# Performance work log

Measured on AMD Instinct MI355X. Metric: run time of the kernel, lower is better.

Reference implementation:

```python
import jax, jax.numpy as jnp
import numpy as np

S, B, D, H, E, K, FF = 1024, 8, 768, 12, 8, 2, 3072


def _ln(x, w, b, eps=1e-5):
    m = x.mean(-1, keepdims=True)
    v = ((x - m) ** 2).mean(-1, keepdims=True)
    return (x - m) / jnp.sqrt(v + eps) * w + b


def setup_inputs() -> dict:
    key = jax.random.key(0)
    ks = jax.random.split(key, 12)
    s = 0.02
    return {
        "x": jax.random.normal(ks[0], (S, B, D), dtype=jnp.float32),
        "ln1_w": jnp.ones((D,), jnp.float32),
        "ln1_b": jnp.zeros((D,), jnp.float32),
        "in_proj_w": jax.random.normal(ks[1], (3 * D, D), jnp.float32) * s,
        "in_proj_b": jnp.zeros((3 * D,), jnp.float32),
        "out_proj_w": jax.random.normal(ks[2], (D, D), jnp.float32) * s,
        "out_proj_b": jnp.zeros((D,), jnp.float32),
        "ln2_w": jnp.ones((D,), jnp.float32),
        "ln2_b": jnp.zeros((D,), jnp.float32),
        "gate_w": jax.random.normal(ks[3], (E, D), jnp.float32) * s,
        "w1": jax.random.normal(ks[4], (E, D, FF), jnp.float32) * s,
        "b1": jnp.zeros((E, FF), jnp.float32),
        "w2": jax.random.normal(ks[5], (E, FF, D), jnp.float32) * s,
        "b2": jnp.zeros((E, D), jnp.float32),
    }


def reference(x, ln1_w, ln1_b, in_proj_w, in_proj_b, out_proj_w, out_proj_b,
              ln2_w, ln2_b, gate_w, w1, b1, w2, b2):
    s, b, d = x.shape
    hd = d // H
    # --- self attention (nn.MultiheadAttention, seq-first, no mask) ---
    h = _ln(x, ln1_w, ln1_b)
    qkv = h @ in_proj_w.T + in_proj_b            # [S, B, 3D]
    q, k, v = jnp.split(qkv, 3, axis=-1)

    def heads(t):
        return t.reshape(s, b, H, hd).transpose(1, 2, 0, 3)  # [B, H, S, hd]

    q, k, v = heads(q) * (hd ** -0.5), heads(k), heads(v)
    att = jax.nn.softmax(jnp.einsum('bhqd,bhkd->bhqk', q, k), axis=-1)
    o = jnp.einsum('bhqk,bhkd->bhqd', att, v).transpose(2, 0, 1, 3).reshape(s, b, d)
    o = o @ out_proj_w.T + out_proj_b
    x = x + o
    # --- MoE FFN ---
    h2 = _ln(x, ln2_w, ln2_b)
    tok = h2.reshape(-1, d)                      # [T, D], T = S*B
    logits = tok @ gate_w.T                      # [T, E]
    rw = jax.nn.softmax(logits.astype(jnp.float32), axis=-1)
    rw_top, sel = jax.lax.top_k(rw, K)           # [T, K]
    rw_top = rw_top / rw_top.sum(-1, keepdims=True)
    rw_top = rw_top.astype(tok.dtype)
    out = jnp.zeros_like(tok)
    for e in range(E):  # small fixed expert loop; math matches gather/scatter dispatch
        we = jnp.where(sel == e, rw_top, 0.0).sum(-1)       # [T] combine weight
        mid = tok @ w1[e] + b1[e]
        mid = mid * jax.nn.sigmoid(1.702 * mid)              # QuickGELU
        out = out + we[:, None] * (mid @ w2[e] + b2[e])
    return x + out.reshape(s, b, d), logits
```

## Files before the change

### kernel.cpp

```cpp
#include <hip/hip_runtime.h>
#include <stdint.h>

#define S_LEN  1024
#define BATCH  8
#define DMODEL 768
#define NHEAD  12
#define HDIM   64
#define NEXP   8
#define FFDIM  3072
#define NTOK   8192
#define D3     2304
#define NGATH  16384
#define MAXWL  136

typedef unsigned short u16;
typedef unsigned int   u32;
typedef __attribute__((ext_vector_type(8))) short bf16x8;
typedef __attribute__((ext_vector_type(4))) float f32x4;
typedef __attribute__((ext_vector_type(4))) short s16x4;

__device__ __forceinline__ u16 f2bf(float f){
  u32 x = __float_as_uint(f);
  x += 0x7fffu + ((x >> 16) & 1u);
  return (u16)(x >> 16);
}
__device__ __forceinline__ float bf2f(u16 u){
  return __uint_as_float(((u32)u) << 16);
}
__device__ __forceinline__ void gl_lds16(const void* g, void* l){
  __builtin_amdgcn_global_load_lds(
      (const __attribute__((address_space(1))) u32*)(uintptr_t)g,
      (__attribute__((address_space(3))) u32*)(u32)(uintptr_t)l,
      16, 0, 0);
}
__device__ __forceinline__ int swz64(int r){ return ((r & 7) ^ ((r >> 3) & 7)) << 4; }

__global__ __launch_bounds__(256)
void cvt_bf16(const float* __restrict__ in, u16* __restrict__ out, int n)
{
  int i = (blockIdx.x * 256 + threadIdx.x) * 4;
  if (i + 3 < n) {
    float4 v = *(const float4*)(in + i);
    out[i]     = f2bf(v.x);
    out[i + 1] = f2bf(v.y);
    out[i + 2] = f2bf(v.z);
    out[i + 3] = f2bf(v.w);
  }
}

__global__ __launch_bounds__(256)
void transpose_cvt(const float* __restrict__ in, u16* __restrict__ out, int rows, int cols)
{
  __shared__ float tile[32][33];
  const size_t eo = (size_t)blockIdx.z * rows * cols;
  in  += eo; out += eo;
  const int bx = blockIdx.x * 32, by = blockIdx.y * 32;
  const int tx = threadIdx.x, ty = threadIdx.y;
  #pragma unroll
  for (int i = 0; i < 4; i++)
    tile[ty + i * 8][tx] = in[(size_t)(by + ty + i * 8) * cols + bx + tx];
  __syncthreads();
  #pragma unroll
  for (int i = 0; i < 4; i++)
    out[(size_t)(bx + ty + i * 8) * rows + by + tx] = f2bf(tile[tx][ty + i * 8]);
}

__global__ __launch_bounds__(256)
void ln_fwd(const float* __restrict__ x, const float* __restrict__ w, const float* __restrict__ b,
            u16* __restrict__ out)
{
  const int t = blockIdx.x, tid = threadIdx.x;
  const float* xr = x + (size_t)t * DMODEL;
  const float v0 = xr[tid], v1 = xr[tid + 256], v2 = xr[tid + 512];
  float s = v0 + v1 + v2, ss = v0 * v0 + v1 * v1 + v2 * v2;
  #pragma unroll
  for (int d = 1; d < 64; d <<= 1) { s += __shfl_xor(s, d); ss += __shfl_xor(ss, d); }
  __shared__ float rs[4], rq[4];
  if ((tid & 63) == 0) { rs[tid >> 6] = s; rq[tid >> 6] = ss; }
  __syncthreads();
  s  = rs[0] + rs[1] + rs[2] + rs[3];
  ss = rq[0] + rq[1] + rq[2] + rq[3];
  const float mean = s * (1.f / DMODEL);
  const float rstd = rsqrtf(ss * (1.f / DMODEL) - mean * mean + 1e-5f);
  u16* orow = out + (size_t)t * DMODEL;
  orow[tid]       = f2bf((v0 - mean) * rstd * w[tid]       + b[tid]);
  orow[tid + 256] = f2bf((v1 - mean) * rstd * w[tid + 256] + b[tid + 256]);
  orow[tid + 512] = f2bf((v2 - mean) * rstd * w[tid + 512] + b[tid + 512]);
}

__global__ __launch_bounds__(256)
void ln2_gate(const float* __restrict__ x1, const float* __restrict__ w, const float* __restrict__ b,
              const float* __restrict__ gate_w, u16* __restrict__ h2,
              float* __restrict__ logits, float* __restrict__ selw, int* __restrict__ seli)
{
  const int t = blockIdx.x, tid = threadIdx.x;
  const float* xr = x1 + (size_t)t * DMODEL;
  const float v0 = xr[tid], v1 = xr[tid + 256], v2 = xr[tid + 512];
  float s = v0 + v1 + v2, ss = v0 * v0 + v1 * v1 + v2 * v2;
  #pragma unroll
  for (int d = 1; d < 64; d <<= 1) { s += __shfl_xor(s, d); ss += __shfl_xor(ss, d); }
  __shared__ float rs[4], rq[4];
  if ((tid & 63) == 0) { rs[tid >> 6] = s; rq[tid >> 6] = ss; }
  __syncthreads();
  s  = rs[0] + rs[1] + rs[2] + rs[3];
  ss = rq[0] + rq[1] + rq[2] + rq[3];
  const float mean = s * (1.f / DMODEL);
  const float rstd = rsqrtf(ss * (1.f / DMODEL) - mean * mean + 1e-5f);
  __shared__ float row[DMODEL];
  const float y0 = (v0 - mean) * rstd * w[tid]       + b[tid];
  const float y1 = (v1 - mean) * rstd * w[tid + 256] + b[tid + 256];
  const float y2 = (v2 - mean) * rstd * w[tid + 512] + b[tid + 512];
  row[tid] = y0; row[tid + 256] = y1; row[tid + 512] = y2;
  u16* hr = h2 + (size_t)t * DMODEL;
  hr[tid] = f2bf(y0); hr[tid + 256] = f2bf(y1); hr[tid + 512] = f2bf(y2);
  __syncthreads();
  __shared__ float lg[NEXP];
  if (tid < 64) {
    const int e = tid >> 3, j = tid & 7;
    const float* gw = gate_w + e * DMODEL;
    float a = 0.f;
    for (int d = j; d < DMODEL; d += 8) a += row[d] * gw[d];
    a += __shfl_xor(a, 1); a += __shfl_xor(a, 2); a += __shfl_xor(a, 4);
    if (j == 0) lg[e] = a;
  }
  __syncthreads();
  if (tid < NEXP) logits[(size_t)t * NEXP + tid] = lg[tid];
  if (tid == 0) {
    int ia = 0, ib = -1;
    float va = -1e30f, vb = -1e30f;
    #pragma unroll
    for (int e = 0; e < NEXP; e++) {
      const float p = lg[e];
      if (p > va)      { vb = va; ib = ia; va = p; ia = e; }
      else if (p > vb) { vb = p; ib = e; }
    }
    const float pb = __expf(vb - va);
    const float inv = 1.f / (1.f + pb);
    selw[2 * t]     = inv;
    selw[2 * t + 1] = pb * inv;
    seli[2 * t]     = ia;
    seli[2 * t + 1] = ib;
  }
}

__global__ __launch_bounds__(256)
void route_count(const int* __restrict__ seli, int* __restrict__ blkcnt)
{
  __shared__ int c[NEXP];
  const int tid = threadIdx.x;
  if (tid < NEXP) c[tid] = 0;
  __syncthreads();
  const int t = blockIdx.x * 256 + tid;
  atomicAdd(&c[seli[2 * t]], 1);
  atomicAdd(&c[seli[2 * t + 1]], 1);
  __syncthreads();
  if (tid < NEXP) blkcnt[blockIdx.x * NEXP + tid] = c[tid];
}

__global__ void route_scan(const int* __restrict__ blkcnt, int* __restrict__ offs,
                           int* __restrict__ blkbase, int* __restrict__ wl, int* __restrict__ nwork)
{
  const int tid = threadIdx.x;
  __shared__ int tot[NEXP];
  __shared__ int off_s[NEXP + 1];
  if (tid < NEXP) {
    int s = 0;
    for (int blk = 0; blk < 32; blk++) s += blkcnt[blk * NEXP + tid];
    tot[tid] = s;
  }
  __syncthreads();
  if (tid == 0) {
    int run = 0;
    for (int e = 0; e < NEXP; e++) { off_s[e] = run; run += tot[e]; }
    off_s[NEXP] = run;
    int nw = 0;
    for (int e = 0; e < NEXP; e++) {
      const int nb = (tot[e] + 127) >> 7;
      for (int i2 = 0; i2 < nb; i2++) wl[nw++] = (e << 16) | i2;
    }
    nwork[0] = nw;
  }
  __syncthreads();
  if (tid <= NEXP) offs[tid] = off_s[tid];
  if (tid < NEXP) {
    int run = off_s[tid];
    for (int blk = 0; blk < 32; blk++) { blkbase[blk * NEXP + tid] = run; run += blkcnt[blk * NEXP + tid]; }
  }
}

__global__ __launch_bounds__(256)
void route_place(const int* __restrict__ seli, const int* __restrict__ blkbase,
                 int* __restrict__ perm, int* __restrict__ posmap)
{
  __shared__ int cnts[2][4][NEXP];
  __shared__ int base[NEXP];
  const int tid = threadIdx.x, l = tid & 63, w = tid >> 6, blk = blockIdx.x;
  const int t = blk * 256 + tid;
  const unsigned long long ltm = (1ull << l) - 1ull;
  int my_e[2], my_r[2];
  my_e[0] = seli[2 * t]; my_e[1] = seli[2 * t + 1];
  my_r[0] = 0; my_r[1] = 0;
  if (tid < NEXP) base[tid] = blkbase[blk * NEXP + tid];
  #pragma unroll
  for (int k = 0; k < 2; k++) {
    #pragma unroll
    for (int ee = 0; ee < NEXP; ee++) {
      const unsigned long long msk = __ballot(my_e[k] == ee);
      if (my_e[k] == ee) my_r[k] = (int)__popcll(msk & ltm);
      if (l == ee) cnts[k][w][ee] = (int)__popcll(msk);
    }
  }
  __syncthreads();
  #pragma unroll
  for (int k = 0; k < 2; k++) {
    const int e = my_e[k];
    int pre = base[e];
    for (int k2 = 0; k2 < 2; k2++)
      for (int w2 = 0; w2 < 4; w2++)
        if (k2 < k || (k2 == k && w2 < w)) pre += cnts[k2][w2][e];
    const int pos = pre + my_r[k];
    perm[pos] = t;
    posmap[2 * t + k] = pos;
  }
}

template<int MODE>
__global__ __launch_bounds__(256)
void gemm128(const u16* __restrict__ A, const u16* __restrict__ Bw,
             int M, int N, int Kd,
             const float* __restrict__ bias, const float* __restrict__ resid,
             void* __restrict__ outp,
             const int* __restrict__ perm, const int* __restrict__ offs,
             const int* __restrict__ wl, const int* __restrict__ nwork)
{
  __shared__ u16 As[128 * 64];
  __shared__ u16 Bs[128 * 64];
  const int tid = threadIdx.x;
  const int l   = tid & 63;
  const int w   = tid >> 6;
  const int wm  = w >> 1, wn = w & 1;
  const int bn  = blockIdx.y;

  int gbase = 0, cnt = M, e = 0, bm = blockIdx.x;
  if (MODE >= 2) {
    if (blockIdx.x >= nwork[0]) return;
    const int wk = wl[blockIdx.x];
    e  = wk >> 16;
    bm = wk & 0xffff;
    gbase = offs[e];
    cnt   = offs[e + 1] - gbase;
  }
  const u16*   Bp = Bw   + (MODE >= 2 ? (size_t)e * N * Kd : 0);
  const float* bp = bias + (MODE >= 2 ? e * N : 0);

  int arow[4], acol[4], brow[4];
  #pragma unroll
  for (int i = 0; i < 4; i++) {
    const int c = tid + 256 * i;
    const int r = c >> 3;
    const int f = (r & 7) ^ ((r >> 3) & 7);
    acol[i] = ((c & 7) ^ f) * 8;
    brow[i] = bn * 128 + r;
    int g;
    if (MODE == 2)      { int gp = gbase + bm * 128 + r; if (gp > NGATH - 1) gp = NGATH - 1; g = perm[gp]; }
    else if (MODE == 3) { int gp = gbase + bm * 128 + r; if (gp > NGATH - 1) gp = NGATH - 1; g = gp; }
    else                g = bm * 128 + r;
    arow[i] = g;
  }

  f32x4 acc[4][4] = {};
  const int nk = Kd >> 6;
  for (int kt = 0; kt < nk; kt++) {
    const int kb = kt * 64;
    #pragma unroll
    for (int i = 0; i < 4; i++) {
      gl_lds16(A  + (size_t)arow[i] * Kd + kb + acol[i], &As[(i * 256 + w * 64) * 8]);
      gl_lds16(Bp + (size_t)brow[i] * Kd + kb + acol[i], &Bs[(i * 256 + w * 64) * 8]);
    }
    __syncthreads();
    #pragma unroll
    for (int ks = 0; ks < 2; ks++) {
      bf16x8 af[4], bv[4];
      #pragma unroll
      for (int m = 0; m < 4; m++) {
        const int row = wm * 64 + m * 16 + (l & 15);
        af[m] = *(const bf16x8*)((const char*)As +
                  ((row * 128 + ks * 64 + (l >> 4) * 16) ^ swz64(row)));
      }
      #pragma unroll
      for (int n = 0; n < 4; n++) {
        const int row = wn * 64 + n * 16 + (l & 15);
        bv[n] = *(const bf16x8*)((const char*)Bs +
                  ((row * 128 + ks * 64 + (l >> 4) * 16) ^ swz64(row)));
      }
      #pragma unroll
      for (int m = 0; m < 4; m++)
        #pragma unroll
        for (int n = 0; n < 4; n++)
          acc[m][n] = __builtin_amdgcn_mfma_f32_16x16x32_bf16(af[m], bv[n], acc[m][n], 0, 0, 0);
    }
    __syncthreads();
  }

  float bvl[4];
  int   coln[4];
  #pragma unroll
  for (int n = 0; n < 4; n++) { coln[n] = bn * 128 + wn * 64 + n * 16 + (l & 15); bvl[n] = bp[coln[n]]; }
  #pragma unroll
  for (int m = 0; m < 4; m++) {
    const int rb = bm * 128 + wm * 64 + m * 16 + ((l >> 4) << 2);
    #pragma unroll
    for (int n = 0; n < 4; n++) {
      #pragma unroll
      for (int r = 0; r < 4; r++) {
        const int row = rb + r;
        const float v = acc[m][n][r] + bvl[n];
        if (MODE == 0) {
          ((u16*)outp)[(size_t)row * N + coln[n]] = f2bf(v);
        } else if (MODE == 1) {
          ((float*)outp)[(size_t)row * N + coln[n]] = v + resid[(size_t)row * N + coln[n]];
        } else if (MODE == 2) {
          if (row < cnt) {
            const float gg = v / (1.f + __expf(-1.702f * v));
            ((u16*)outp)[(size_t)(gbase + row) * FFDIM + coln[n]] = f2bf(gg);
          }
        } else {
          if (row < cnt)
            ((u16*)outp)[(size_t)(gbase + row) * DMODEL + coln[n]] = f2bf(v);
        }
      }
    }
  }
}

__global__ __launch_bounds__(256)
void attn_fwd(const u16* __restrict__ qkv, u16* __restrict__ o)
{
  __shared__ u16 Ksw[64 * 64];
  __shared__ u16 Vt [64 * 64];
  __shared__ u16 Pl [4 * 16 * 64];
  const int tid = threadIdx.x;
  const int l   = tid & 63, w = tid >> 6;
  const int qt  = blockIdx.x;
  const int b_  = blockIdx.y / NHEAD;
  const int hh  = blockIdx.y % NHEAD;

  const int qrow = qt * 64 + w * 16 + (l & 15);
  const size_t qoff = ((size_t)(qrow * BATCH + b_)) * D3 + hh * HDIM + (l >> 4) * 8;
  const bf16x8 qa0 = *(const bf16x8*)&qkv[qoff];
  const bf16x8 qa1 = *(const bf16x8*)&qkv[qoff + 32];

  f32x4 oacc[4] = {};
  float m_[4], l_[4];
  #pragma unroll
  for (int r = 0; r < 4; r++) { m_[r] = -1e30f; l_[r] = 0.f; }

  u16* Pw = Pl + w * 1024;
  const int pswz = swz64(l & 15);

  for (int kt = 0; kt < 16; kt++) {
    #pragma unroll
    for (int i = 0; i < 2; i++) {
      const int c = tid + 256 * i;
      const int key = c >> 3, dimb = (c & 7) * 8;
      const size_t gb = ((size_t)((kt * 64 + key) * BATCH + b_)) * D3 + hh * HDIM + dimb;
      const bf16x8 kd = *(const bf16x8*)&qkv[gb + DMODEL];
      const bf16x8 vd = *(const bf16x8*)&qkv[gb + 2 * DMODEL];
      *(bf16x8*)((char*)Ksw + ((key * 128 + dimb * 2) ^ swz64(key))) = kd;
      #pragma unroll
      for (int j = 0; j < 8; j++) {
        const int dim = dimb + j;
        *(u16*)((char*)Vt + ((dim * 128 + key * 2) ^ swz64(dim))) = (u16)vd[j];
      }
    }
    __syncthreads();

    f32x4 sc[4] = {};
    #pragma unroll
    for (int kb2 = 0; kb2 < 4; kb2++) {
      const int key = kb2 * 16 + (l & 15);
      const int ksz = swz64(key);
      #pragma unroll
      for (int ks = 0; ks < 2; ks++) {
        const bf16x8 kf = *(const bf16x8*)((char*)Ksw +
            ((key * 128 + (ks * 32 + (l >> 4) * 8) * 2) ^ ksz));
        sc[kb2] = __builtin_amdgcn_mfma_f32_16x16x32_bf16(ks ? qa1 : qa0, kf, sc[kb2], 0, 0, 0);
      }
    }
    #pragma unroll
    for (int kb2 = 0; kb2 < 4; kb2++)
      #pragma unroll
      for (int r = 0; r < 4; r++) sc[kb2][r] *= 0.125f;

    float nm[4], corr[4], ps[4];
    #pragma unroll
    for (int r = 0; r < 4; r++) {
      float pm = fmaxf(fmaxf(sc[0][r], sc[1][r]), fmaxf(sc[2][r], sc[3][r]));
      pm = fmaxf(pm, __shfl_xor(pm, 1));
      pm = fmaxf(pm, __shfl_xor(pm, 2));
      pm = fmaxf(pm, __shfl_xor(pm, 4));
      pm = fmaxf(pm, __shfl_xor(pm, 8));
      nm[r]   = fmaxf(m_[r], pm);
      corr[r] = __expf(m_[r] - nm[r]);
      m_[r]   = nm[r];
      ps[r]   = 0.f;
    }
    #pragma unroll
    for (int kb2 = 0; kb2 < 4; kb2++) {
      #pragma unroll
      for (int r = 0; r < 4; r++) {
        const float p = __expf(sc[kb2][r] - nm[r]);
        ps[r] += p;
        const int prow = (l >> 4) * 4 + r;
        const int pcol = kb2 * 16 + (l & 15);
        *(u16*)((char*)Pw + ((prow * 128 + pcol * 2) ^ swz64(prow))) = f2bf(p);
      }
    }
    #pragma unroll
    for (int r = 0; r < 4; r++) {
      float s = ps[r];
      s += __shfl_xor(s, 1); s += __shfl_xor(s, 2);
      s += __shfl_xor(s, 4); s += __shfl_xor(s, 8);
      l_[r] = l_[r] * corr[r] + s;
      #pragma unroll
      for (int ob = 0; ob < 4; ob++) oacc[ob][r] *= corr[r];
    }

    #pragma unroll
    for (int ob = 0; ob < 4; ob++) {
      const int dim = ob * 16 + (l & 15);
      const int vsz = swz64(dim);
      #pragma unroll
      for (int ks = 0; ks < 2; ks++) {
        const int kko = (ks * 32 + (l >> 4) * 8) * 2;
        const bf16x8 pf = *(const bf16x8*)((char*)Pw + (((l & 15) * 128 + kko) ^ pswz));
        const bf16x8 vf = *(const bf16x8*)((char*)Vt + ((dim * 128 + kko) ^ vsz));
        oacc[ob] = __builtin_amdgcn_mfma_f32_16x16x32_bf16(pf, vf, oacc[ob], 0, 0, 0);
      }
    }
    __syncthreads();
  }

  #pragma unroll
  for (int r = 0; r < 4; r++) {
    const float inv = 1.f / l_[r];
    const int qs = qt * 64 + w * 16 + (l >> 4) * 4 + r;
    #pragma unroll
    for (int ob = 0; ob < 4; ob++)
      o[((size_t)(qs * BATCH + b_)) * DMODEL + hh * HDIM + ob * 16 + (l & 15)] =
          f2bf(oacc[ob][r] * inv);
  }
}

__global__ __launch_bounds__(192)
void moe_combine(const float* __restrict__ x1, const u16* __restrict__ eout,
                 const int* __restrict__ posmap, const float* __restrict__ selw,
                 float* __restrict__ out)
{
  const int t = blockIdx.x, j = threadIdx.x;
  const int p0 = posmap[2 * t], p1 = posmap[2 * t + 1];
  const float w0 = selw[2 * t], w1 = selw[2 * t + 1];
  const float4 xv = ((const float4*)(x1 + (size_t)t * DMODEL))[j];
  const s16x4 a = ((const s16x4*)(eout + (size_t)p0 * DMODEL))[j];
  const s16x4 c = ((const s16x4*)(eout + (size_t)p1 * DMODEL))[j];
  float4 r;
  r.x = xv.x + w0 * bf2f((u16)a[0]) + w1 * bf2f((u16)c[0]);
  r.y = xv.y + w0 * bf2f((u16)a[1]) + w1 * bf2f((u16)c[1]);
  r.z = xv.z + w0 * bf2f((u16)a[2]) + w1 * bf2f((u16)c[2]);
  r.w = xv.w + w0 * bf2f((u16)a[3]) + w1 * bf2f((u16)c[3]);
  ((float4*)(out + (size_t)t * DMODEL))[j] = r;
}

#define MB (1ull << 20)
static const size_t OFF_H    = 0;
static const size_t OFF_QKV  = 16 * MB;
static const size_t OFF_O    = 54 * MB;
static const size_t OFF_IPW  = 67 * MB;
static const size_t OFF_OPW  = 71 * MB;
static const size_t OFF_MID  = 0;
static const size_t OFF_X1   = 101 * MB;
static const size_t OFF_H2   = 127 * MB;
static const size_t OFF_W1T  = 140 * MB;
static const size_t OFF_W2T  = 178 * MB;
static const size_t OFF_EOUT = 216 * MB;
static const size_t OFF_SELW = 242 * MB;
static const size_t OFF_PERM = 242 * MB + (1 << 16);
static const size_t OFF_POS  = 242 * MB + (2 << 16);
static const size_t OFF_SELI = 242 * MB + (3 << 16);
static const size_t OFF_BCNT = 242 * MB + (4 << 16);
static const size_t OFF_BBASE= 242 * MB + (4 << 16) + 4096;
static const size_t OFF_OFFS = 242 * MB + (4 << 16) + 8192;
static const size_t OFF_WL   = 242 * MB + (5 << 16);
static const size_t OFF_NW   = 242 * MB + (5 << 16) + 1024;

extern "C" void kernel_launch(void* const* d_in, const int* in_sizes, int n_in,
                              void* d_out, int out_size, void* d_ws, size_t ws_size,
                              hipStream_t stream)
{
  const float* x     = (const float*)d_in[0];
  const float* ln1w  = (const float*)d_in[1];
  const float* ln1b  = (const float*)d_in[2];
  const float* ipw_f = (const float*)d_in[3];
  const float* ipb   = (const float*)d_in[4];
  const float* opw_f = (const float*)d_in[5];
  const float* opb   = (const float*)d_in[6];
  const float* ln2w  = (const float*)d_in[7];
  const float* ln2b  = (const float*)d_in[8];
  const float* gatew = (const float*)d_in[9];
  const float* w1    = (const float*)d_in[10];
  const float* b1    = (const float*)d_in[11];
  const float* w2    = (const float*)d_in[12];
  const float* b2    = (const float*)d_in[13];

  char* ws = (char*)d_ws;
  u16*   h    = (u16*)(ws + OFF_H);
  u16*   qkv  = (u16*)(ws + OFF_QKV);
  u16*   ob   = (u16*)(ws + OFF_O);
  u16*   ipw  = (u16*)(ws + OFF_IPW);
  u16*   opw  = (u16*)(ws + OFF_OPW);
  u16*   mid  = (u16*)(ws + OFF_MID);
  float* x1   = (float*)(ws + OFF_X1);
  u16*   h2   = (u16*)(ws + OFF_H2);
  u16*   w1t  = (u16*)(ws + OFF_W1T);
  u16*   w2t  = (u16*)(ws + OFF_W2T);
  u16*   eout = (u16*)(ws + OFF_EOUT);
  float* selw = (float*)(ws + OFF_SELW);
  int*   perm = (int*)(ws + OFF_PERM);
  int*   posm = (int*)(ws + OFF_POS);
  int*   seli = (int*)(ws + OFF_SELI);
  int*   bcnt = (int*)(ws + OFF_BCNT);
  int*   bbas = (int*)(ws + OFF_BBASE);
  int*   offs = (int*)(ws + OFF_OFFS);
  int*   wl   = (int*)(ws + OFF_WL);
  int*   nwork= (int*)(ws + OFF_NW);
  float* outx  = (float*)d_out;
  float* outlg = outx + (size_t)NTOK * DMODEL;

  cvt_bf16<<<(D3 * DMODEL) / 1024, 256, 0, stream>>>(ipw_f, ipw, D3 * DMODEL);
  cvt_bf16<<<(DMODEL * DMODEL) / 1024, 256, 0, stream>>>(opw_f, opw, DMODEL * DMODEL);
  transpose_cvt<<<dim3(FFDIM / 32, DMODEL / 32, NEXP), dim3(32, 8), 0, stream>>>(w1, w1t, DMODEL, FFDIM);
  transpose_cvt<<<dim3(DMODEL / 32, FFDIM / 32, NEXP), dim3(32, 8), 0, stream>>>(w2, w2t, FFDIM, DMODEL);

  ln_fwd<<<NTOK, 256, 0, stream>>>(x, ln1w, ln1b, h);
  gemm128<0><<<dim3(NTOK / 128, D3 / 128, 1), 256, 0, stream>>>(
      h, ipw, NTOK, D3, DMODEL, ipb, nullptr, qkv, nullptr, nullptr, nullptr, nullptr);
  attn_fwd<<<dim3(S_LEN / 64, BATCH * NHEAD), 256, 0, stream>>>(qkv, ob);
  gemm128<1><<<dim3(NTOK / 128, DMODEL / 128, 1), 256, 0, stream>>>(
      ob, opw, NTOK, DMODEL, DMODEL, opb, x, x1, nullptr, nullptr, nullptr, nullptr);

  ln2_gate<<<NTOK, 256, 0, stream>>>(x1, ln2w, ln2b, gatew, h2, outlg, selw, seli);
  route_count<<<32, 256, 0, stream>>>(seli, bcnt);
  route_scan<<<1, 64, 0, stream>>>(bcnt, offs, bbas, wl, nwork);
  route_place<<<32, 256, 0, stream>>>(seli, bbas, perm, posm);

  gemm128<2><<<dim3(MAXWL, FFDIM / 128, 1), 256, 0, stream>>>(
      h2, w1t, NGATH, FFDIM, DMODEL, b1, nullptr, mid, perm, offs, wl, nwork);
  gemm128<3><<<dim3(MAXWL, DMODEL / 128, 1), 256, 0, stream>>>(
      mid, w2t, NGATH, DMODEL, FFDIM, b2, nullptr, eout, nullptr, offs, wl, nwork);

  moe_combine<<<NTOK, 192, 0, stream>>>(x1, eout, posm, selw, outx);
}
```

Baseline: 594.7 us.

## Enlarge GEMM tiles to 256x128 and vectorize epilogue stores

Doubles the M dimension of every GEMM block tile to 256 rows, so each warp computes a 128x64 sub-tile with 32 accumulators. Routing work lists are rebuilt in 256-row chunks to match, which halves the block count and the B-tile reloads. MFMA operands are swapped so each lane holds four consecutive output columns, which lets the epilogue use packed bf16 conversion and vector stores, and bias and residual become vector loads. The costs are higher register and LDS use, lower occupancy, and more padded rows wasted in the expert GEMMs.

```diff
diff --git a/kernel.cpp b/kernel.cpp
--- a/kernel.cpp
+++ b/kernel.cpp
@@ -11,7 +11,7 @@
 #define NTOK   8192
 #define D3     2304
 #define NGATH  16384
-#define MAXWL  136
+#define MAXWL  72
 
 typedef unsigned short u16;
 typedef unsigned int   u32;
@@ -26,6 +26,9 @@
 }
 __device__ __forceinline__ float bf2f(u16 u){
   return __uint_as_float(((u32)u) << 16);
+}
+__device__ __forceinline__ u32 pkbf(float a, float b){
+  u32 d; asm("v_cvt_pk_bf16_f32 %0, %1, %2" : "=v"(d) : "v"(a), "v"(b)); return d;
 }
 __device__ __forceinline__ void gl_lds16(const void* g, void* l){
   __builtin_amdgcn_global_load_lds(
@@ -175,7 +178,7 @@
     off_s[NEXP] = run;
     int nw = 0;
     for (int e = 0; e < NEXP; e++) {
-      const int nb = (tot[e] + 127) >> 7;
+      const int nb = (tot[e] + 255) >> 8;
       for (int i2 = 0; i2 < nb; i2++) wl[nw++] = (e << 16) | i2;
     }
     nwork[0] = nw;
@@ -226,14 +229,14 @@
 
 template<int MODE>
 __global__ __launch_bounds__(256)
-void gemm128(const u16* __restrict__ A, const u16* __restrict__ Bw,
+void gemm256(const u16* __restrict__ A, const u16* __restrict__ Bw,
              int M, int N, int Kd,
              const float* __restrict__ bias, const float* __restrict__ resid,
              void* __restrict__ outp,
              const int* __restrict__ perm, const int* __restrict__ offs,
              const int* __restrict__ wl, const int* __restrict__ nwork)
 {
-  __shared__ u16 As[128 * 64];
+  __shared__ u16 As[256 * 64];
   __shared__ u16 Bs[128 * 64];
   const int tid = threadIdx.x;
   const int l   = tid & 63;
@@ -253,40 +256,35 @@
   const u16*   Bp = Bw   + (MODE >= 2 ? (size_t)e * N * Kd : 0);
   const float* bp = bias + (MODE >= 2 ? e * N : 0);
 
-  int arow[4], acol[4], brow[4];
-  #pragma unroll
-  for (int i = 0; i < 4; i++) {
+  int arow[8], acol[8], brow[4];
+  #pragma unroll
+  for (int i = 0; i < 8; i++) {
     const int c = tid + 256 * i;
     const int r = c >> 3;
     const int f = (r & 7) ^ ((r >> 3) & 7);
     acol[i] = ((c & 7) ^ f) * 8;
-    brow[i] = bn * 128 + r;
     int g;
-    if (MODE == 2)      { int gp = gbase + bm * 128 + r; if (gp > NGATH - 1) gp = NGATH - 1; g = perm[gp]; }
-    else if (MODE == 3) { int gp = gbase + bm * 128 + r; if (gp > NGATH - 1) gp = NGATH - 1; g = gp; }
-    else                g = bm * 128 + r;
+    if (MODE == 2)      { int gp = gbase + bm * 256 + r; if (gp > NGATH - 1) gp = NGATH - 1; g = perm[gp]; }
+    else if (MODE == 3) { int gp = gbase + bm * 256 + r; if (gp > NGATH - 1) gp = NGATH - 1; g = gp; }
+    else                g = bm * 256 + r;
     arow[i] = g;
-  }
-
-  f32x4 acc[4][4] = {};
+    if (i < 4) brow[i] = bn * 128 + r;
+  }
+
+  f32x4 acc[8][4] = {};
   const int nk = Kd >> 6;
   for (int kt = 0; kt < nk; kt++) {
     const int kb = kt * 64;
     #pragma unroll
-    for (int i = 0; i < 4; i++) {
-      gl_lds16(A  + (size_t)arow[i] * Kd + kb + acol[i], &As[(i * 256 + w * 64) * 8]);
-      gl_lds16(Bp + (size_t)brow[i] * Kd + kb + acol[i], &Bs[(i * 256 + w * 64) * 8]);
+    for (int i = 0; i < 8; i++) {
+      gl_lds16(A + (size_t)arow[i] * Kd + kb + acol[i], &As[(tid + 256 * i) * 8]);
+      if (i < 4)
+        gl_lds16(Bp + (size_t)brow[i] * Kd + kb + acol[i], &Bs[(tid + 256 * i) * 8]);
     }
     __syncthreads();
     #pragma unroll
     for (int ks = 0; ks < 2; ks++) {
-      bf16x8 af[4], bv[4];
-      #pragma unroll
-      for (int m = 0; m < 4; m++) {
-        const int row = wm * 64 + m * 16 + (l & 15);
-        af[m] = *(const bf16x8*)((const char*)As +
-                  ((row * 128 + ks * 64 + (l >> 4) * 16) ^ swz64(row)));
-      }
+      bf16x8 bv[4];
       #pragma unroll
       for (int n = 0; n < 4; n++) {
         const int row = wn * 64 + n * 16 + (l & 15);
@@ -294,40 +292,51 @@
                   ((row * 128 + ks * 64 + (l >> 4) * 16) ^ swz64(row)));
       }
       #pragma unroll
-      for (int m = 0; m < 4; m++)
+      for (int m = 0; m < 8; m++) {
+        const int row = wm * 128 + m * 16 + (l & 15);
+        const bf16x8 af = *(const bf16x8*)((const char*)As +
+                  ((row * 128 + ks * 64 + (l >> 4) * 16) ^ swz64(row)));
         #pragma unroll
         for (int n = 0; n < 4; n++)
-          acc[m][n] = __builtin_amdgcn_mfma_f32_16x16x32_bf16(af[m], bv[n], acc[m][n], 0, 0, 0);
+          acc[m][n] = __builtin_amdgcn_mfma_f32_16x16x32_bf16(bv[n], af, acc[m][n], 0, 0, 0);
+      }
     }
     __syncthreads();
   }
 
-  float bvl[4];
-  int   coln[4];
-  #pragma unroll
-  for (int n = 0; n < 4; n++) { coln[n] = bn * 128 + wn * 64 + n * 16 + (l & 15); bvl[n] = bp[coln[n]]; }
-  #pragma unroll
-  for (int m = 0; m < 4; m++) {
-    const int rb = bm * 128 + wm * 64 + m * 16 + ((l >> 4) << 2);
+  f32x4 biasv[4];
+  int   c0[4];
+  #pragma unroll
+  for (int n = 0; n < 4; n++) {
+    c0[n] = bn * 128 + wn * 64 + n * 16 + ((l >> 4) << 2);
+    biasv[n] = *(const f32x4*)(bp + c0[n]);
+  }
+  #pragma unroll
+  for (int m = 0; m < 8; m++) {
+    const int row = bm * 256 + wm * 128 + m * 16 + (l & 15);
     #pragma unroll
     for (int n = 0; n < 4; n++) {
-      #pragma unroll
-      for (int r = 0; r < 4; r++) {
-        const int row = rb + r;
-        const float v = acc[m][n][r] + bvl[n];
-        if (MODE == 0) {
-          ((u16*)outp)[(size_t)row * N + coln[n]] = f2bf(v);
-        } else if (MODE == 1) {
-          ((float*)outp)[(size_t)row * N + coln[n]] = v + resid[(size_t)row * N + coln[n]];
-        } else if (MODE == 2) {
-          if (row < cnt) {
-            const float gg = v / (1.f + __expf(-1.702f * v));
-            ((u16*)outp)[(size_t)(gbase + row) * FFDIM + coln[n]] = f2bf(gg);
-          }
-        } else {
-          if (row < cnt)
-            ((u16*)outp)[(size_t)(gbase + row) * DMODEL + coln[n]] = f2bf(v);
+      f32x4 v = acc[m][n] + biasv[n];
+      if (MODE == 0) {
+        *(uint2*)((u16*)outp + (size_t)row * N + c0[n]) =
+            make_uint2(pkbf(v[0], v[1]), pkbf(v[2], v[3]));
+      } else if (MODE == 1) {
+        const size_t o = (size_t)row * N + c0[n];
+        f32x4 rv = *(const f32x4*)(resid + o);
+        v += rv;
+        *(f32x4*)((float*)outp + o) = v;
+      } else if (MODE == 2) {
+        if (row < cnt) {
+          #pragma unroll
+          for (int r = 0; r < 4; r++)
+            v[r] = v[r] * __builtin_amdgcn_rcpf(1.f + __expf(-1.702f * v[r]));
+          *(uint2*)((u16*)outp + (size_t)(gbase + row) * FFDIM + c0[n]) =
+              make_uint2(pkbf(v[0], v[1]), pkbf(v[2], v[3]));
         }
+      } else {
+        if (row < cnt)
+          *(uint2*)((u16*)outp + (size_t)(gbase + row) * DMODEL + c0[n]) =
+              make_uint2(pkbf(v[0], v[1]), pkbf(v[2], v[3]));
       }
     }
   }
@@ -542,10 +551,10 @@
   transpose_cvt<<<dim3(DMODEL / 32, FFDIM / 32, NEXP), dim3(32, 8), 0, stream>>>(w2, w2t, FFDIM, DMODEL);
 
   ln_fwd<<<NTOK, 256, 0, stream>>>(x, ln1w, ln1b, h);
-  gemm128<0><<<dim3(NTOK / 128, D3 / 128, 1), 256, 0, stream>>>(
+  gemm256<0><<<dim3(NTOK / 256, D3 / 128, 1), 256, 0, stream>>>(
       h, ipw, NTOK, D3, DMODEL, ipb, nullptr, qkv, nullptr, nullptr, nullptr, nullptr);
   attn_fwd<<<dim3(S_LEN / 64, BATCH * NHEAD), 256, 0, stream>>>(qkv, ob);
-  gemm128<1><<<dim3(NTOK / 128, DMODEL / 128, 1), 256, 0, stream>>>(
+  gemm256<1><<<dim3(NTOK / 256, DMODEL / 128, 1), 256, 0, stream>>>(
       ob, opw, NTOK, DMODEL, DMODEL, opb, x, x1, nullptr, nullptr, nullptr, nullptr);
 
   ln2_gate<<<NTOK, 256, 0, stream>>>(x1, ln2w, ln2b, gatew, h2, outlg, selw, seli);
@@ -553,9 +562,9 @@
   route_scan<<<1, 64, 0, stream>>>(bcnt, offs, bbas, wl, nwork);
   route_place<<<32, 256, 0, stream>>>(seli, bbas, perm, posm);
 
-  gemm128<2><<<dim3(MAXWL, FFDIM / 128, 1), 256, 0, stream>>>(
+  gemm256<2><<<dim3(MAXWL, FFDIM / 128, 1), 256, 0, stream>>>(
       h2, w1t, NGATH, FFDIM, DMODEL, b1, nullptr, mid, perm, offs, wl, nwork);
-  gemm128<3><<<dim3(MAXWL, DMODEL / 128, 1), 256, 0, stream>>>(
+  gemm256<3><<<dim3(MAXWL, DMODEL / 128, 1), 256, 0, stream>>>(
       mid, w2t, NGATH, DMODEL, FFDIM, b2, nullptr, eout, nullptr, offs, wl, nwork);
 
   moe_combine<<<NTOK, 192, 0, stream>>>(x1, eout, posm, selw, outx);
```

New measurement: 732.0 us. 23.1% more time.
